# Kernel optimization log

Hardware: AMD Instinct MI355X
Metric: run time of the kernel (lower is better)

## Reference

```python
import jax, jax.numpy as jnp
import numpy as np

MID = 16
HEADS = 8
HEAD_DIM = MID // HEADS  # 2
EPS = 1e-5


def posembed(length, dim):
    # get_posembed_linear: sin-cos 1D positional embedding
    pos = jnp.arange(length, dtype=jnp.float32)
    omega = jnp.arange(dim // 2, dtype=jnp.float32) / (dim / 2.0)
    omega = 1.0 / (10000.0 ** omega)
    out = pos[:, None] * omega[None, :]  # [L, dim//2]
    return jnp.concatenate([jnp.sin(out), jnp.cos(out)], axis=1)  # [L, dim]


def layernorm(x, g, b):
    m = x.mean(-1, keepdims=True)
    v = ((x - m) ** 2).mean(-1, keepdims=True)
    return (x - m) * jax.lax.rsqrt(v + EPS) * g + b


def conv2d(x, w, b):
    # NCHW 3x3 SAME conv
    y = jax.lax.conv_general_dilated(x, w, (1, 1), 'SAME',
                                     dimension_numbers=('NCHW', 'OIHW', 'NCHW'))
    return y + b[None, :, None, None]


def attention(x, wq, wk, wv, wo, bo):
    # diffusers Attention: self-attn, no qkv bias, out bias
    B, S, C = x.shape
    q = (x @ wq.T).reshape(B, S, HEADS, HEAD_DIM)
    k = (x @ wk.T).reshape(B, S, HEADS, HEAD_DIM)
    v = (x @ wv.T).reshape(B, S, HEADS, HEAD_DIM)
    scale = 1.0 / np.sqrt(HEAD_DIM).astype(np.float32)
    scores = jnp.einsum('bshd,bthd->bhst', q, k) * scale
    p = jax.nn.softmax(scores, axis=-1)
    o = jnp.einsum('bhst,bthd->bshd', p, v).reshape(B, S, C)
    return o @ wo.T + bo


def setup_inputs() -> dict:
    key = jax.random.key(0)
    ks = jax.random.split(key, 24)

    def n(k, shape, s=0.05):
        return jax.random.normal(k, shape, dtype=jnp.float32) * s

    b, f, h, w, c = 2, 16, 64, 64, 16
    inp = {
        'hidden_states': n(ks[0], (b, f, h, w, c), 1.0),
        'ref_stats': n(ks[1], (b, f, h, w, c), 1.0),
        'emb': n(ks[2], (b, 512), 1.0),
        'conv_in_w': n(ks[3], (MID, c, 3, 3)),
        'conv_in_b': jnp.zeros((MID,), jnp.float32),
        'emb1_w': n(ks[4], (MID, 512)),
        'emb1_b': jnp.zeros((MID,), jnp.float32),
        'emb2_w': n(ks[5], (MID, MID)),
        'emb2_b': jnp.zeros((MID,), jnp.float32),
        'wqx': n(ks[6], (MID, MID)), 'wkx': n(ks[7], (MID, MID)),
        'wvx': n(ks[8], (MID, MID)), 'wox': n(ks[9], (MID, MID)),
        'box': jnp.zeros((MID,), jnp.float32),
        'wqy': n(ks[10], (MID, MID)), 'wky': n(ks[11], (MID, MID)),
        'wvy': n(ks[12], (MID, MID)), 'woy': n(ks[13], (MID, MID)),
        'boy': jnp.zeros((MID,), jnp.float32),
        'wqt': n(ks[14], (MID, MID)), 'wkt': n(ks[15], (MID, MID)),
        'wvt': n(ks[16], (MID, MID)), 'wot': n(ks[17], (MID, MID)),
        'bot': jnp.zeros((MID,), jnp.float32),
        'norm_g': jnp.ones((MID,), jnp.float32),
        'norm_b': jnp.zeros((MID,), jnp.float32),
        'proj_w': n(ks[18], (c, MID, 3, 3)),  # zero_module in torch; random here so grads flow
        'proj_b': jnp.zeros((c,), jnp.float32),
    }
    return inp


def reference(hidden_states, ref_stats, emb,
              conv_in_w, conv_in_b, emb1_w, emb1_b, emb2_w, emb2_b,
              wqx, wkx, wvx, wox, box,
              wqy, wky, wvy, woy, boy,
              wqt, wkt, wvt, wot, bot,
              norm_g, norm_b, proj_w, proj_b):
    b, f, h, w, c = hidden_states.shape

    # conv stem on (b f) c h w
    x = hidden_states.reshape(b * f, h, w, c).transpose(0, 3, 1, 2)
    x = conv2d(x, conv_in_w, conv_in_b)
    r = ref_stats.reshape(b * f, h, w, c).transpose(0, 3, 1, 2)
    r = conv2d(r, conv_in_w, conv_in_b)

    # TimestepEmbedding: linear -> silu -> linear, broadcast over frames/HW
    e = jax.nn.silu(emb @ emb1_w.T + emb1_b) @ emb2_w.T + emb2_b  # [b, MID]
    r = r + jnp.repeat(e, f, axis=0)[:, :, None, None]

    hs = x.reshape(b, f, MID, h, w).transpose(0, 1, 3, 4, 2)  # b f h w c
    rs = r.reshape(b, f, MID, h, w).transpose(0, 1, 3, 4, 2)

    # row (x) attention: cat along w -> (b f h) 2w c
    cat = jnp.concatenate([hs, rs], axis=3).reshape(b * f * h, 2 * w, MID)
    pe = posembed(2 * w, MID)
    resx = attention(layernorm(cat + pe[None], norm_g, norm_b), wqx, wkx, wvx, wox, box)
    resx = resx[:, :w].reshape(b, f, h, w, MID)

    # column (y) attention: cat along h -> (b f w) 2h c
    cat = jnp.concatenate([resx, rs], axis=2)            # b f 2h w c
    cat = cat.transpose(0, 1, 3, 2, 4).reshape(b * f * w, 2 * h, MID)
    pe = posembed(2 * h, MID)
    resy = attention(layernorm(cat + pe[None], norm_g, norm_b), wqy, wky, wvy, woy, boy)
    resy = resy[:, :h].reshape(b, f, w, h, MID).transpose(0, 1, 3, 2, 4)

    # temporal (t) attention: cat along f -> (b h w) 2f c
    cat = jnp.concatenate([resy, rs], axis=1)            # b 2f h w c
    cat = cat.transpose(0, 2, 3, 1, 4).reshape(b * h * w, 2 * f, MID)
    pe = posembed(2 * f, MID)
    rest = attention(layernorm(cat + pe[None], norm_g, norm_b), wqt, wkt, wvt, wot, bot)
    rest = rest[:, :f].reshape(b, h, w, f, MID).transpose(0, 3, 4, 1, 2).reshape(b * f, MID, h, w)

    out = conv2d(rest, proj_w, proj_b)  # (b f) c h w
    return hidden_states + out.reshape(b, f, c, h, w).transpose(0, 1, 3, 4, 2)
```

## Files before the change

kernel.cpp:

```cpp
#include <hip/hip_runtime.h>
#include <hip/hip_bf16.h>

typedef __hip_bfloat16 bf16;
using hf2 = decltype(__builtin_amdgcn_cvt_pkrtz(0.f, 0.f));
typedef float f32x2 __attribute__((ext_vector_type(2)));
typedef _Float16 v4h __attribute__((ext_vector_type(4)));
typedef float v4f __attribute__((ext_vector_type(4)));

#define BB   2
#define FF   16
#define HH   64
#define WW   64
#define CC   16
#define NIMG (BB*FF)
#define PIX  (HH*WW)
#define IMGSZ (PIX*CC)

#define QSCALE_LOG2E 1.0201394f

__device__ __forceinline__ unsigned pkh2(float a, float b) {
    union { hf2 h; unsigned u; } x;
    x.h = __builtin_amdgcn_cvt_pkrtz(a, b);
    return x.u;
}
__device__ __forceinline__ float fdot2u(unsigned a, unsigned b, float c) {
    union { unsigned u; hf2 h; } A, B;
    A.u = a; B.u = b;
    return __builtin_amdgcn_fdot2(A.h, B.h, c, false);
}
__device__ __forceinline__ f32x2 f2(float a, float b) {
    f32x2 r; r.x = a; r.y = b; return r;
}

__device__ __forceinline__ void ld16f(const float* p, float* x) {
    const float4* p4 = reinterpret_cast<const float4*>(p);
    #pragma unroll
    for (int q = 0; q < 4; ++q) {
        float4 v = p4[q];
        x[4 * q] = v.x; x[4 * q + 1] = v.y; x[4 * q + 2] = v.z; x[4 * q + 3] = v.w;
    }
}

__device__ __forceinline__ unsigned packbf2(float a, float b) {
    union { bf16 h[2]; unsigned u; } pk;
    pk.h[0] = __float2bfloat16(a);
    pk.h[1] = __float2bfloat16(b);
    return pk.u;
}

__device__ __forceinline__ void stage_wB(const float* __restrict__ w,
                                         unsigned* __restrict__ wB, int t) {
    for (int e = t; e < 576; e += 256) {
        int oc = e & 15;
        int c  = (e >> 4) & 3;
        int s  = e >> 6;
        const float* wp = w + (oc * 16 + c * 4) * 9 + s;
        wB[e * 2]     = pkh2(wp[0],  wp[9]);
        wB[e * 2 + 1] = pkh2(wp[18], wp[27]);
    }
}

#define TAP_OFF(s) ((((s) / 3) * 66 + ((s) % 3)) * 12)

__global__ __launch_bounds__(256) void conv_in_kernel(
    const float* __restrict__ hid, const float* __restrict__ ref,
    const float* __restrict__ cw, const float* __restrict__ cb,
    const float* __restrict__ emb,
    const float* __restrict__ e1w, const float* __restrict__ e1b,
    const float* __restrict__ e2w, const float* __restrict__ e2b,
    bf16* __restrict__ A, bf16* __restrict__ R)
{
    __shared__ __align__(16) unsigned stg[6 * 66 * 12];
    __shared__ __align__(16) unsigned wB[1152];
    __shared__ float bl[16], hl[16], el[16];

    int t = threadIdx.x;
    int bid = blockIdx.x;
    int rg   = bid & 15;
    int img2 = bid >> 4;
    int isref = img2 >> 5;
    int img   = img2 & 31;
    int bi    = img >> 4;
    int r0    = rg << 2;

    stage_wB(cw, wB, t);
    if (t < 16) bl[t] = cb[t];

    if (isref) {
        float* red = reinterpret_cast<float*>(stg);
        {
            int o = t >> 4, seg = t & 15;
            const float* er = emb + bi * 512 + seg * 32;
            const float* wr = e1w + o * 512 + seg * 32;
            float p = 0.f;
            #pragma unroll
            for (int k = 0; k < 32; ++k) p = fmaf(er[k], wr[k], p);
            red[t] = p;
        }
        __syncthreads();
        if (t < 16) {
            float acc = e1b[t];
            #pragma unroll
            for (int s = 0; s < 16; ++s) acc += red[t * 16 + s];
            hl[t] = acc / (1.f + __expf(-acc));
        }
        __syncthreads();
        if (t < 16) {
            float acc = e2b[t];
            #pragma unroll
            for (int k = 0; k < 16; ++k) acc = fmaf(hl[k], e2w[t * 16 + k], acc);
            el[t] = acc;
        }
        __syncthreads();
    }

    const float* inp = (isref ? ref : hid) + (size_t)img * IMGSZ;
    for (int s2 = t; s2 < 396; s2 += 256) {
        int rr = s2 / 66, xi = s2 - rr * 66;
        int y = r0 - 1 + rr, px = xi - 1;
        uint4* dst = reinterpret_cast<uint4*>(&stg[(rr * 66 + xi) * 12]);
        if ((unsigned)y < 64u && (unsigned)px < 64u) {
            float xv[16];
            ld16f(inp + (((y << 6) + px) << 4), xv);
            dst[0] = make_uint4(pkh2(xv[0], xv[1]),  pkh2(xv[2], xv[3]),
                                pkh2(xv[4], xv[5]),  pkh2(xv[6], xv[7]));
            dst[1] = make_uint4(pkh2(xv[8], xv[9]),  pkh2(xv[10], xv[11]),
                                pkh2(xv[12], xv[13]), pkh2(xv[14], xv[15]));
        } else {
            dst[0] = make_uint4(0, 0, 0, 0);
            dst[1] = make_uint4(0, 0, 0, 0);
        }
    }
    __syncthreads();

    int l  = t & 63, w = t >> 6;
    int oc = l & 15, c = l >> 4;
    int y  = r0 + w;

    v4h bf[9];
    int cb2 = c * 32 + oc * 2;
    #pragma unroll
    for (int s = 0; s < 9; ++s)
        bf[s] = *reinterpret_cast<const v4h*>(&wB[s * 128 + cb2]);

    float bias = bl[oc] + (isref ? el[oc] : 0.f);
    v4f binit; binit[0] = bias; binit[1] = bias; binit[2] = bias; binit[3] = bias;

    bf16* op = (isref ? R : A) + (size_t)img * IMGSZ;

    #pragma unroll
    for (int xq = 0; xq < 4; ++xq) {
        int ab = (w * 66 + xq * 16 + (l & 15)) * 12 + 2 * c;
        v4f acc = binit;
        #pragma unroll
        for (int s = 0; s < 9; ++s) {
            v4h af = *reinterpret_cast<const v4h*>(&stg[ab + TAP_OFF(s)]);
            acc = __builtin_amdgcn_mfma_f32_16x16x16f16(af, bf[s], acc, 0, 0, 0);
        }
        #pragma unroll
        for (int g = 0; g < 4; ++g) {
            int x = xq * 16 + c * 4 + g;
            op[(((y << 6) + x) << 4) + oc] = __float2bfloat16(acc[g]);
        }
    }
}

template<int S, int SEQPB, int MINW, bool F16OUT>
__global__ __launch_bounds__(256, MINW) void attn_kernel(
    bf16* __restrict__ A, const bf16* __restrict__ R,
    unsigned* __restrict__ A16,
    int d2, int str1, int str2, int tokStride,
    const float* __restrict__ wq, const float* __restrict__ wk,
    const float* __restrict__ wv, const float* __restrict__ wo,
    const float* __restrict__ bo, const float* __restrict__ gw,
    const float* __restrict__ bw)
{
    constexpr int HS  = S / 2;
    constexpr int KQ  = S / 2;
    constexpr int TPT = 256 / (SEQPB * S);
    static_assert(TPT == 2, "all stages use the pair-thread layout");
    constexpr int ITEMS = 256 / SEQPB;
    constexpr int NQG = ITEMS / 16;
    constexpr int QB  = HS / NQG;
    constexpr int QP  = QB / 2;
    constexpr int KROW = 10;
    constexpr int QROW = 20;
    constexpr int KTROW = S + 12;
    constexpr int LSQ = (SEQPB == 1) ? 0 : ((SEQPB == 2) ? 1 : 2);
    constexpr int NW3 = SEQPB * HS * 8 / 256;

    __shared__ float wolT[256];
    __shared__ unsigned wq2L[128], wk2L[128], wv2L[128];
    __shared__ float bol[16], gl[16], blw[16];
    __shared__ __align__(16) unsigned kvT[2 * SEQPB * 8 * KTROW];
    __shared__ __align__(16) unsigned qL[SEQPB * HS * KROW];
    __shared__ int bases[SEQPB];
    unsigned* kT = kvT;
    unsigned* vT = kvT + SEQPB * 8 * KTROW;

    int t = threadIdx.x;
    wolT[(t & 15) * 16 + (t >> 4)] = wo[t];
    if (t < 128) {
        float2 qw = reinterpret_cast<const float2*>(wq)[t];
        float2 kw = reinterpret_cast<const float2*>(wk)[t];
        float2 vw = reinterpret_cast<const float2*>(wv)[t];
        wq2L[t] = pkh2(qw.x * QSCALE_LOG2E, qw.y * QSCALE_LOG2E);
        wk2L[t] = pkh2(kw.x, kw.y);
        wv2L[t] = pkh2(vw.x, vw.y);
    }
    if (t < 16) { bol[t] = bo[t]; gl[t] = gw[t]; blw[t] = bw[t]; }
    if (t < SEQPB) {
        int seq = blockIdx.x * SEQPB + t;
        bases[t] = (seq / d2) * str1 + (seq % d2) * str2;
    }
    __syncthreads();

    const float om[8] = {1.f, 0.31622776601683794f, 0.1f, 0.031622776601683794f,
                         0.01f, 0.0031622776601683794f, 0.001f, 0.00031622776601683794f};

    {
        int tokIdx = t >> 1;
        int half = t & 1;
        int db   = half * 8;
        int sq = tokIdx & (SEQPB - 1);
        int i  = tokIdx >> LSQ;
        const bf16* src = ((i < HS)
            ? (A + bases[sq] + (size_t)i * tokStride)
            : (R + bases[sq] + (size_t)(i - HS) * tokStride)) + db;
        uint4 u = *reinterpret_cast<const uint4*>(src);
        unsigned uu[4] = {u.x, u.y, u.z, u.w};
        float x[8];
        #pragma unroll
        for (int k = 0; k < 4; ++k) {
            union { unsigned u; float f; } lo, hi2;
            lo.u = uu[k] << 16; hi2.u = uu[k] & 0xffff0000u;
            x[2 * k] = lo.f; x[2 * k + 1] = hi2.f;
        }
        float fi = (float)i;
        #pragma unroll
        for (int k = 0; k < 8; ++k) {
            float sv, cv;
            __sincosf(fi * om[k], &sv, &cv);
            x[k] += half ? cv : sv;
        }
        float s8 = 0.f;
        #pragma unroll
        for (int k = 0; k < 8; ++k) s8 += x[k];
        float m = (s8 + __shfl_xor(s8, 1)) * (1.f / 16.f);
        float v8 = 0.f;
        #pragma unroll
        for (int k = 0; k < 8; ++k) { float d = x[k] - m; v8 = fmaf(d, d, v8); }
        float var = (v8 + __shfl_xor(v8, 1)) * (1.f / 16.f);
        float rs = rsqrtf(var + 1e-5f);

        unsigned xpm[4];
        #pragma unroll
        for (int e = 0; e < 4; ++e) {
            float a0 = (x[2 * e]     - m) * rs * gl[db + 2 * e]     + blw[db + 2 * e];
            float a1 = (x[2 * e + 1] - m) * rs * gl[db + 2 * e + 1] + blw[db + 2 * e + 1];
            xpm[e] = pkh2(a0, a1);
        }
        unsigned xp[8];
        #pragma unroll
        for (int e = 0; e < 4; ++e) {
            unsigned oth = __shfl_xor(xpm[e], 1);
            xp[e]     = half ? oth    : xpm[e];
            xp[e + 4] = half ? xpm[e] : oth;
        }
        float qv[8], kv[8], vv[8];
        #pragma unroll
        for (int dd = 0; dd < 8; ++dd) {
            int d = db + dd;
            float aq = 0.f, ak = 0.f, av = 0.f;
            #pragma unroll
            for (int c2 = 0; c2 < 8; ++c2) {
                aq = fdot2u(xp[c2], wq2L[d * 8 + c2], aq);
                ak = fdot2u(xp[c2], wk2L[d * 8 + c2], ak);
                av = fdot2u(xp[c2], wv2L[d * 8 + c2], av);
            }
            qv[dd] = aq; kv[dd] = ak; vv[dd] = av;
        }
        int hb = db >> 1;
        #pragma unroll
        for (int e = 0; e < 4; ++e) {
            int hrow = (sq * 8 + hb + e) * KTROW + i;
            kT[hrow] = pkh2(kv[2 * e], kv[2 * e + 1]);
            vT[hrow] = packbf2(vv[2 * e], vv[2 * e + 1]);
        }
        if (i < HS) {
            uint2* qr = reinterpret_cast<uint2*>(&qL[(sq * HS + i) * KROW + (db >> 1)]);
            #pragma unroll
            for (int e = 0; e < 2; ++e)
                qr[e] = make_uint2(pkh2(qv[4 * e], qv[4 * e + 1]),
                                   pkh2(qv[4 * e + 2], qv[4 * e + 3]));
        }
    }
    __syncthreads();

    int sq2 = t / ITEMS;
    int r   = t % ITEMS;
    int qg  = r >> 4;
    int hd  = (r >> 1) & 7;
    int half2 = r & 1;
    float* oL = reinterpret_cast<float*>(kvT);
    {
        unsigned q2[QB];
        f32x2 l2[QP], a0p[QP], a1p[QP];
        #pragma unroll
        for (int qq = 0; qq < QB; ++qq)
            q2[qq] = qL[(sq2 * HS + qg * QB + qq) * KROW + hd];
        #pragma unroll
        for (int m = 0; m < QP; ++m) {
            l2[m] = f2(0.f, 0.f); a0p[m] = f2(0.f, 0.f); a1p[m] = f2(0.f, 0.f);
        }
        const unsigned* kp = &kT[(sq2 * 8 + hd) * KTROW + half2 * KQ];
        const unsigned* vp = &vT[(sq2 * 8 + hd) * KTROW + half2 * KQ];
        #pragma unroll 4
        for (int jb = 0; jb < KQ / 4; ++jb) {
            uint4 k4 = *reinterpret_cast<const uint4*>(kp + jb * 4);
            uint4 v4 = *reinterpret_cast<const uint4*>(vp + jb * 4);
            unsigned ks[4] = {k4.x, k4.y, k4.z, k4.w};
            unsigned vs[4] = {v4.x, v4.y, v4.z, v4.w};
            #pragma unroll
            for (int e = 0; e < 4; ++e) {
                union { unsigned u; float f; } v0, v1;
                v0.u = vs[e] << 16; v1.u = vs[e] & 0xffff0000u;
                f32x2 v00 = f2(v0.f, v0.f);
                f32x2 v11 = f2(v1.f, v1.f);
                #pragma unroll
                for (int m = 0; m < QP; ++m) {
                    f32x2 p2;
                    p2.x = __builtin_amdgcn_exp2f(fdot2u(q2[2 * m], ks[e], 0.f));
                    p2.y = __builtin_amdgcn_exp2f(fdot2u(q2[2 * m + 1], ks[e], 0.f));
                    l2[m] += p2;
                    a0p[m] = __builtin_elementwise_fma(p2, v00, a0p[m]);
                    a1p[m] = __builtin_elementwise_fma(p2, v11, a1p[m]);
                }
            }
        }
        #pragma unroll
        for (int m = 0; m < QP; ++m) {
            l2[m].x  += __shfl_xor(l2[m].x, 1);  l2[m].y  += __shfl_xor(l2[m].y, 1);
            a0p[m].x += __shfl_xor(a0p[m].x, 1); a0p[m].y += __shfl_xor(a0p[m].y, 1);
            a1p[m].x += __shfl_xor(a1p[m].x, 1); a1p[m].y += __shfl_xor(a1p[m].y, 1);
        }
        __syncthreads();
        if (half2 == 0) {
            #pragma unroll
            for (int m = 0; m < QP; ++m) {
                float inv0 = 1.f / l2[m].x;
                float inv1 = 1.f / l2[m].y;
                *reinterpret_cast<float2*>(
                    &oL[(sq2 * HS + qg * QB + 2 * m) * QROW + 2 * hd]) =
                    make_float2(a0p[m].x * inv0, a1p[m].x * inv0);
                *reinterpret_cast<float2*>(
                    &oL[(sq2 * HS + qg * QB + 2 * m + 1) * QROW + 2 * hd]) =
                    make_float2(a0p[m].y * inv1, a1p[m].y * inv1);
            }
        }
    }
    __syncthreads();

    #pragma unroll
    for (int rep = 0; rep < NW3; ++rep) {
        int idx = t + rep * 256;
        int cp  = idx & 7;
        int g   = idx >> 3;
        int sq3 = g & (SEQPB - 1);
        int tok = g >> LSQ;
        const float* orow = &oL[(sq3 * HS + tok) * QROW];
        float acc0 = bol[2 * cp], acc1 = bol[2 * cp + 1];
        #pragma unroll
        for (int d = 0; d < 16; ++d) {
            acc0 = fmaf(orow[d], wolT[d * 16 + 2 * cp], acc0);
            acc1 = fmaf(orow[d], wolT[d * 16 + 2 * cp + 1], acc1);
        }
        int off = bases[sq3] + tok * tokStride;
        if constexpr (F16OUT)
            A16[(off >> 1) + cp] = pkh2(acc0, acc1);
        else
            *reinterpret_cast<unsigned*>(A + off + 2 * cp) = packbf2(acc0, acc1);
    }
}

__global__ __launch_bounds__(256) void conv_out_kernel(
    const unsigned* __restrict__ A16, const float* __restrict__ hid,
    const float* __restrict__ pw, const float* __restrict__ pb,
    float* __restrict__ out)
{
    __shared__ __align__(16) unsigned stg[4 * 66 * 12];
    __shared__ __align__(16) unsigned wB[1152];
    __shared__ float bl[16];

    int t = threadIdx.x;
    int bid = blockIdx.x;
    int rg  = bid & 31;
    int img = bid >> 5;
    int r0  = rg << 1;

    stage_wB(pw, wB, t);
    if (t < 16) bl[t] = pb[t];

    const unsigned* inp = A16 + ((size_t)img << 15);
    for (int s2 = t; s2 < 264; s2 += 256) {
        int rr = s2 / 66, xi = s2 - rr * 66;
        int y = r0 - 1 + rr, px = xi - 1;
        uint4* dst = reinterpret_cast<uint4*>(&stg[(rr * 66 + xi) * 12]);
        if ((unsigned)y < 64u && (unsigned)px < 64u) {
            const uint4* sp = reinterpret_cast<const uint4*>(
                inp + (((y << 6) + px) << 3));
            dst[0] = sp[0];
            dst[1] = sp[1];
        } else {
            dst[0] = make_uint4(0, 0, 0, 0);
            dst[1] = make_uint4(0, 0, 0, 0);
        }
    }
    __syncthreads();

    int l  = t & 63, w = t >> 6;
    int oc = l & 15, c = l >> 4;

    v4h bf[9];
    int cb2 = c * 32 + oc * 2;
    #pragma unroll
    for (int s = 0; s < 9; ++s)
        bf[s] = *reinterpret_cast<const v4h*>(&wB[s * 128 + cb2]);

    float bias = bl[oc];
    v4f binit; binit[0] = bias; binit[1] = bias; binit[2] = bias; binit[3] = bias;
    size_t obase = (size_t)img * IMGSZ;

    #pragma unroll
    for (int tq = 0; tq < 2; ++tq) {
        int tile = w * 2 + tq;
        int ro = tile >> 2, xq = tile & 3;
        int y  = r0 + ro;
        int ab = (ro * 66 + xq * 16 + (l & 15)) * 12 + 2 * c;
        v4f acc = binit;
        #pragma unroll
        for (int s = 0; s < 9; ++s) {
            v4h af = *reinterpret_cast<const v4h*>(&stg[ab + TAP_OFF(s)]);
            acc = __builtin_amdgcn_mfma_f32_16x16x16f16(af, bf[s], acc, 0, 0, 0);
        }
        #pragma unroll
        for (int g = 0; g < 4; ++g) {
            int x = xq * 16 + c * 4 + g;
            size_t o = obase + (size_t)(((y << 6) + x) << 4) + oc;
            out[o] = acc[g] + hid[o];
        }
    }
}

extern "C" void kernel_launch(void* const* d_in, const int* in_sizes, int n_in,
                              void* d_out, int out_size, void* d_ws, size_t ws_size,
                              hipStream_t stream) {
    const float* hid  = (const float*)d_in[0];
    const float* ref  = (const float*)d_in[1];
    const float* emb  = (const float*)d_in[2];
    const float* ciw  = (const float*)d_in[3];
    const float* cib  = (const float*)d_in[4];
    const float* e1w  = (const float*)d_in[5];
    const float* e1b  = (const float*)d_in[6];
    const float* e2w  = (const float*)d_in[7];
    const float* e2b  = (const float*)d_in[8];
    const float* wqx  = (const float*)d_in[9];
    const float* wkx  = (const float*)d_in[10];
    const float* wvx  = (const float*)d_in[11];
    const float* wox  = (const float*)d_in[12];
    const float* box_ = (const float*)d_in[13];
    const float* wqy  = (const float*)d_in[14];
    const float* wky  = (const float*)d_in[15];
    const float* wvy  = (const float*)d_in[16];
    const float* woy  = (const float*)d_in[17];
    const float* boy  = (const float*)d_in[18];
    const float* wqt  = (const float*)d_in[19];
    const float* wkt  = (const float*)d_in[20];
    const float* wvt  = (const float*)d_in[21];
    const float* wot  = (const float*)d_in[22];
    const float* bot  = (const float*)d_in[23];
    const float* ng   = (const float*)d_in[24];
    const float* nb   = (const float*)d_in[25];
    const float* pjw  = (const float*)d_in[26];
    const float* pjb  = (const float*)d_in[27];

    bf16* A = (bf16*)d_ws;
    unsigned* A16 = (unsigned*)((char*)d_ws + (4 << 20));
    bf16* R = (bf16*)d_out;

    conv_in_kernel<<<2 * NIMG * (HH / 4), 256, 0, stream>>>(
        hid, ref, ciw, cib, emb, e1w, e1b, e2w, e2b, A, R);

    attn_kernel<128, 1, 8, false><<<BB * FF * HH, 256, 0, stream>>>(
        A, R, nullptr, 1, WW * CC, 0, CC, wqx, wkx, wvx, wox, box_, ng, nb);
    attn_kernel<128, 1, 8, false><<<BB * FF * WW, 256, 0, stream>>>(
        A, R, nullptr, WW, IMGSZ, CC, WW * CC, wqy, wky, wvy, woy, boy, ng, nb);
    attn_kernel<32, 4, 8, true><<<(BB * HH * WW) / 4, 256, 0, stream>>>(
        A, R, A16, HH * WW, FF * IMGSZ, CC, IMGSZ, wqt, wkt, wvt, wot, bot, ng, nb);

    conv_out_kernel<<<NIMG * (HH / 2), 256, 0, stream>>>(
        A16, hid, pjw, pjb, (float*)d_out);
}
```

Measured before the change: 224.7 us.

## Fuse input conv and row attention into a single per-row kernel

Merges the conv_in kernel with the x-direction (row) attention stage. Each block convolves one image row of both hidden and reference inputs into LDS as fp16 tokens, then runs layernorm, QKV projection, softmax attention and the output projection in place. The A buffer no longer has to be written and read back from global memory, and one launch goes away. In exchange, each block recomputes the embedding MLP, and the input halo rows are loaded about three times instead of about 1.5 times, since each block now covers one row rather than four.

```diff
diff --git a/kernel.cpp b/kernel.cpp
--- a/kernel.cpp
+++ b/kernel.cpp
@@ -30,6 +30,10 @@
 }
 __device__ __forceinline__ f32x2 f2(float a, float b) {
     f32x2 r; r.x = a; r.y = b; return r;
+}
+__device__ __forceinline__ void unpkh(unsigned u, float& a, float& b) {
+    union { unsigned v; __fp16 h[2]; } x; x.v = u;
+    a = (float)x.h[0]; b = (float)x.h[1];
 }
 
 __device__ __forceinline__ void ld16f(const float* p, float* x) {
@@ -62,106 +66,280 @@
 
 #define TAP_OFF(s) ((((s) / 3) * 66 + ((s) % 3)) * 12)
 
-__global__ __launch_bounds__(256) void conv_in_kernel(
+__global__ __launch_bounds__(256, 6) void cx_kernel(
     const float* __restrict__ hid, const float* __restrict__ ref,
     const float* __restrict__ cw, const float* __restrict__ cb,
     const float* __restrict__ emb,
     const float* __restrict__ e1w, const float* __restrict__ e1b,
     const float* __restrict__ e2w, const float* __restrict__ e2b,
-    bf16* __restrict__ A, bf16* __restrict__ R)
+    bf16* __restrict__ A, bf16* __restrict__ R,
+    const float* __restrict__ wq, const float* __restrict__ wk,
+    const float* __restrict__ wv, const float* __restrict__ wo,
+    const float* __restrict__ bo, const float* __restrict__ gw,
+    const float* __restrict__ bw)
 {
-    __shared__ __align__(16) unsigned stg[6 * 66 * 12];
+    constexpr int HS = 64, KQ = 64;
+    constexpr int QB = 4, QP = 2;
+    constexpr int KROW = 10;
+    constexpr int QROW = 20;
+    constexpr int KTROW = 140;
+
+    __shared__ __align__(16) unsigned stgU[2376];
+    __shared__ __align__(16) unsigned tokL[1024];
     __shared__ __align__(16) unsigned wB[1152];
-    __shared__ float bl[16], hl[16], el[16];
+    __shared__ unsigned wq2L[128], wk2L[128], wv2L[128];
+    __shared__ float wolT[256];
+    __shared__ float bol[16], gl[16], blw[16], bl[16], hl[16], el[16];
 
     int t = threadIdx.x;
-    int bid = blockIdx.x;
-    int rg   = bid & 15;
-    int img2 = bid >> 4;
-    int isref = img2 >> 5;
-    int img   = img2 & 31;
-    int bi    = img >> 4;
-    int r0    = rg << 2;
+    int seq = blockIdx.x;
+    int h   = seq & 63;
+    int img = seq >> 6;
+    int bi  = seq >> 10;
+    int base = img * IMGSZ + h * (WW * CC);
 
     stage_wB(cw, wB, t);
-    if (t < 16) bl[t] = cb[t];
-
-    if (isref) {
-        float* red = reinterpret_cast<float*>(stg);
-        {
-            int o = t >> 4, seg = t & 15;
-            const float* er = emb + bi * 512 + seg * 32;
-            const float* wr = e1w + o * 512 + seg * 32;
-            float p = 0.f;
-            #pragma unroll
-            for (int k = 0; k < 32; ++k) p = fmaf(er[k], wr[k], p);
-            red[t] = p;
-        }
-        __syncthreads();
-        if (t < 16) {
-            float acc = e1b[t];
-            #pragma unroll
-            for (int s = 0; s < 16; ++s) acc += red[t * 16 + s];
-            hl[t] = acc / (1.f + __expf(-acc));
-        }
-        __syncthreads();
-        if (t < 16) {
-            float acc = e2b[t];
-            #pragma unroll
-            for (int k = 0; k < 16; ++k) acc = fmaf(hl[k], e2w[t * 16 + k], acc);
-            el[t] = acc;
-        }
-        __syncthreads();
-    }
-
-    const float* inp = (isref ? ref : hid) + (size_t)img * IMGSZ;
-    for (int s2 = t; s2 < 396; s2 += 256) {
-        int rr = s2 / 66, xi = s2 - rr * 66;
-        int y = r0 - 1 + rr, px = xi - 1;
-        uint4* dst = reinterpret_cast<uint4*>(&stg[(rr * 66 + xi) * 12]);
-        if ((unsigned)y < 64u && (unsigned)px < 64u) {
-            float xv[16];
-            ld16f(inp + (((y << 6) + px) << 4), xv);
-            dst[0] = make_uint4(pkh2(xv[0], xv[1]),  pkh2(xv[2], xv[3]),
-                                pkh2(xv[4], xv[5]),  pkh2(xv[6], xv[7]));
-            dst[1] = make_uint4(pkh2(xv[8], xv[9]),  pkh2(xv[10], xv[11]),
-                                pkh2(xv[12], xv[13]), pkh2(xv[14], xv[15]));
-        } else {
-            dst[0] = make_uint4(0, 0, 0, 0);
-            dst[1] = make_uint4(0, 0, 0, 0);
-        }
-    }
-    __syncthreads();
+    wolT[(t & 15) * 16 + (t >> 4)] = wo[t];
+    if (t < 128) {
+        float2 qw = reinterpret_cast<const float2*>(wq)[t];
+        float2 kw = reinterpret_cast<const float2*>(wk)[t];
+        float2 vw = reinterpret_cast<const float2*>(wv)[t];
+        wq2L[t] = pkh2(qw.x * QSCALE_LOG2E, qw.y * QSCALE_LOG2E);
+        wk2L[t] = pkh2(kw.x, kw.y);
+        wv2L[t] = pkh2(vw.x, vw.y);
+    }
+    if (t < 16) { bol[t] = bo[t]; gl[t] = gw[t]; blw[t] = bw[t]; bl[t] = cb[t]; }
+
+    {
+        float* red = reinterpret_cast<float*>(tokL);
+        int o = t >> 4, seg = t & 15;
+        const float* er = emb + bi * 512 + seg * 32;
+        const float* wr = e1w + o * 512 + seg * 32;
+        float p = 0.f;
+        #pragma unroll
+        for (int k = 0; k < 32; ++k) p = fmaf(er[k], wr[k], p);
+        red[t] = p;
+    }
+    __syncthreads();
+    if (t < 16) {
+        float* red = reinterpret_cast<float*>(tokL);
+        float acc = e1b[t];
+        #pragma unroll
+        for (int s = 0; s < 16; ++s) acc += red[t * 16 + s];
+        hl[t] = acc / (1.f + __expf(-acc));
+    }
+    __syncthreads();
+    if (t < 16) {
+        float acc = e2b[t];
+        #pragma unroll
+        for (int k = 0; k < 16; ++k) acc = fmaf(hl[k], e2w[t * 16 + k], acc);
+        el[t] = acc;
+    }
 
     int l  = t & 63, w = t >> 6;
     int oc = l & 15, c = l >> 4;
-    int y  = r0 + w;
-
-    v4h bf[9];
-    int cb2 = c * 32 + oc * 2;
+    v4h bfr[9];
+    {
+        int cb2 = c * 32 + oc * 2;
+        #pragma unroll
+        for (int s = 0; s < 9; ++s)
+            bfr[s] = *reinterpret_cast<const v4h*>(&wB[s * 128 + cb2]);
+    }
+    __fp16* tok16 = reinterpret_cast<__fp16*>(tokL);
+
     #pragma unroll
-    for (int s = 0; s < 9; ++s)
-        bf[s] = *reinterpret_cast<const v4h*>(&wB[s * 128 + cb2]);
-
-    float bias = bl[oc] + (isref ? el[oc] : 0.f);
-    v4f binit; binit[0] = bias; binit[1] = bias; binit[2] = bias; binit[3] = bias;
-
-    bf16* op = (isref ? R : A) + (size_t)img * IMGSZ;
+    for (int pass = 0; pass < 2; ++pass) {
+        __syncthreads();
+        const float* inp = (pass ? ref : hid) + (size_t)img * IMGSZ;
+        for (int s2 = t; s2 < 198; s2 += 256) {
+            int rr = s2 / 66, xi = s2 - rr * 66;
+            int y = h - 1 + rr, px = xi - 1;
+            uint4* dst = reinterpret_cast<uint4*>(&stgU[(rr * 66 + xi) * 12]);
+            if ((unsigned)y < 64u && (unsigned)px < 64u) {
+                float xv[16];
+                ld16f(inp + (((y << 6) + px) << 4), xv);
+                dst[0] = make_uint4(pkh2(xv[0], xv[1]),  pkh2(xv[2], xv[3]),
+                                    pkh2(xv[4], xv[5]),  pkh2(xv[6], xv[7]));
+                dst[1] = make_uint4(pkh2(xv[8], xv[9]),  pkh2(xv[10], xv[11]),
+                                    pkh2(xv[12], xv[13]), pkh2(xv[14], xv[15]));
+            } else {
+                dst[0] = make_uint4(0, 0, 0, 0);
+                dst[1] = make_uint4(0, 0, 0, 0);
+            }
+        }
+        __syncthreads();
+
+        float bias = bl[oc] + (pass ? el[oc] : 0.f);
+        v4f acc; acc[0] = bias; acc[1] = bias; acc[2] = bias; acc[3] = bias;
+        int ab = ((w << 4) + (l & 15)) * 12 + 2 * c;
+        #pragma unroll
+        for (int s = 0; s < 9; ++s) {
+            v4h af = *reinterpret_cast<const v4h*>(&stgU[ab + TAP_OFF(s)]);
+            acc = __builtin_amdgcn_mfma_f32_16x16x16f16(af, bfr[s], acc, 0, 0, 0);
+        }
+        #pragma unroll
+        for (int g = 0; g < 4; ++g) {
+            int px = (w << 4) + (c << 2) + g;
+            tok16[(pass * 64 + px) * 16 + oc] = (__fp16)acc[g];
+            if (pass)
+                R[base + px * CC + oc] = __float2bfloat16(acc[g]);
+        }
+    }
+    __syncthreads();
+
+    unsigned* kT = stgU;
+    unsigned* vT = stgU + 8 * KTROW;
+
+    const float om[8] = {1.f, 0.31622776601683794f, 0.1f, 0.031622776601683794f,
+                         0.01f, 0.0031622776601683794f, 0.001f, 0.00031622776601683794f};
+
+    __shared__ __align__(16) unsigned qL[HS * KROW];
+    {
+        int i    = t >> 1;
+        int half = t & 1;
+        int db   = half * 8;
+        uint4 u = *reinterpret_cast<const uint4*>(&tokL[i * 8 + half * 4]);
+        unsigned uu[4] = {u.x, u.y, u.z, u.w};
+        float x[8];
+        #pragma unroll
+        for (int k = 0; k < 4; ++k) unpkh(uu[k], x[2 * k], x[2 * k + 1]);
+        float fi = (float)i;
+        #pragma unroll
+        for (int k = 0; k < 8; ++k) {
+            float sv, cv;
+            __sincosf(fi * om[k], &sv, &cv);
+            x[k] += half ? cv : sv;
+        }
+        float s8 = 0.f;
+        #pragma unroll
+        for (int k = 0; k < 8; ++k) s8 += x[k];
+        float m = (s8 + __shfl_xor(s8, 1)) * (1.f / 16.f);
+        float v8 = 0.f;
+        #pragma unroll
+        for (int k = 0; k < 8; ++k) { float d = x[k] - m; v8 = fmaf(d, d, v8); }
+        float var = (v8 + __shfl_xor(v8, 1)) * (1.f / 16.f);
+        float rs = rsqrtf(var + 1e-5f);
+
+        unsigned xpm[4];
+        #pragma unroll
+        for (int e = 0; e < 4; ++e) {
+            float a0 = (x[2 * e]     - m) * rs * gl[db + 2 * e]     + blw[db + 2 * e];
+            float a1 = (x[2 * e + 1] - m) * rs * gl[db + 2 * e + 1] + blw[db + 2 * e + 1];
+            xpm[e] = pkh2(a0, a1);
+        }
+        unsigned xp[8];
+        #pragma unroll
+        for (int e = 0; e < 4; ++e) {
+            unsigned oth = __shfl_xor(xpm[e], 1);
+            xp[e]     = half ? oth    : xpm[e];
+            xp[e + 4] = half ? xpm[e] : oth;
+        }
+        float qv[8], kv[8], vv[8];
+        #pragma unroll
+        for (int dd = 0; dd < 8; ++dd) {
+            int d = db + dd;
+            float aq = 0.f, ak = 0.f, av = 0.f;
+            #pragma unroll
+            for (int c2 = 0; c2 < 8; ++c2) {
+                aq = fdot2u(xp[c2], wq2L[d * 8 + c2], aq);
+                ak = fdot2u(xp[c2], wk2L[d * 8 + c2], ak);
+                av = fdot2u(xp[c2], wv2L[d * 8 + c2], av);
+            }
+            qv[dd] = aq; kv[dd] = ak; vv[dd] = av;
+        }
+        int hb = db >> 1;
+        #pragma unroll
+        for (int e = 0; e < 4; ++e) {
+            int hrow = (hb + e) * KTROW + i;
+            kT[hrow] = pkh2(kv[2 * e], kv[2 * e + 1]);
+            vT[hrow] = packbf2(vv[2 * e], vv[2 * e + 1]);
+        }
+        if (i < HS) {
+            uint2* qr = reinterpret_cast<uint2*>(&qL[i * KROW + (db >> 1)]);
+            #pragma unroll
+            for (int e = 0; e < 2; ++e)
+                qr[e] = make_uint2(pkh2(qv[4 * e], qv[4 * e + 1]),
+                                   pkh2(qv[4 * e + 2], qv[4 * e + 3]));
+        }
+    }
+    __syncthreads();
+
+    int qg  = t >> 4;
+    int hd  = (t >> 1) & 7;
+    int half2 = t & 1;
+    float* oL = reinterpret_cast<float*>(stgU);
+    {
+        unsigned q2[QB];
+        f32x2 l2[QP], a0p[QP], a1p[QP];
+        #pragma unroll
+        for (int qq = 0; qq < QB; ++qq)
+            q2[qq] = qL[(qg * QB + qq) * KROW + hd];
+        #pragma unroll
+        for (int m = 0; m < QP; ++m) {
+            l2[m] = f2(0.f, 0.f); a0p[m] = f2(0.f, 0.f); a1p[m] = f2(0.f, 0.f);
+        }
+        const unsigned* kp = &kT[hd * KTROW + half2 * KQ];
+        const unsigned* vp = &vT[hd * KTROW + half2 * KQ];
+        #pragma unroll 4
+        for (int jb = 0; jb < KQ / 4; ++jb) {
+            uint4 k4 = *reinterpret_cast<const uint4*>(kp + jb * 4);
+            uint4 v4 = *reinterpret_cast<const uint4*>(vp + jb * 4);
+            unsigned ks[4] = {k4.x, k4.y, k4.z, k4.w};
+            unsigned vs[4] = {v4.x, v4.y, v4.z, v4.w};
+            #pragma unroll
+            for (int e = 0; e < 4; ++e) {
+                union { unsigned u; float f; } v0, v1;
+                v0.u = vs[e] << 16; v1.u = vs[e] & 0xffff0000u;
+                f32x2 v00 = f2(v0.f, v0.f);
+                f32x2 v11 = f2(v1.f, v1.f);
+                #pragma unroll
+                for (int m = 0; m < QP; ++m) {
+                    f32x2 p2;
+                    p2.x = __builtin_amdgcn_exp2f(fdot2u(q2[2 * m], ks[e], 0.f));
+                    p2.y = __builtin_amdgcn_exp2f(fdot2u(q2[2 * m + 1], ks[e], 0.f));
+                    l2[m] += p2;
+                    a0p[m] = __builtin_elementwise_fma(p2, v00, a0p[m]);
+                    a1p[m] = __builtin_elementwise_fma(p2, v11, a1p[m]);
+                }
+            }
+        }
+        #pragma unroll
+        for (int m = 0; m < QP; ++m) {
+            l2[m].x  += __shfl_xor(l2[m].x, 1);  l2[m].y  += __shfl_xor(l2[m].y, 1);
+            a0p[m].x += __shfl_xor(a0p[m].x, 1); a0p[m].y += __shfl_xor(a0p[m].y, 1);
+            a1p[m].x += __shfl_xor(a1p[m].x, 1); a1p[m].y += __shfl_xor(a1p[m].y, 1);
+        }
+        __syncthreads();
+        if (half2 == 0) {
+            #pragma unroll
+            for (int m = 0; m < QP; ++m) {
+                float inv0 = 1.f / l2[m].x;
+                float inv1 = 1.f / l2[m].y;
+                *reinterpret_cast<float2*>(
+                    &oL[(qg * QB + 2 * m) * QROW + 2 * hd]) =
+                    make_float2(a0p[m].x * inv0, a1p[m].x * inv0);
+                *reinterpret_cast<float2*>(
+                    &oL[(qg * QB + 2 * m + 1) * QROW + 2 * hd]) =
+                    make_float2(a0p[m].y * inv1, a1p[m].y * inv1);
+            }
+        }
+    }
+    __syncthreads();
 
     #pragma unroll
-    for (int xq = 0; xq < 4; ++xq) {
-        int ab = (w * 66 + xq * 16 + (l & 15)) * 12 + 2 * c;
-        v4f acc = binit;
-        #pragma unroll
-        for (int s = 0; s < 9; ++s) {
-            v4h af = *reinterpret_cast<const v4h*>(&stg[ab + TAP_OFF(s)]);
-            acc = __builtin_amdgcn_mfma_f32_16x16x16f16(af, bf[s], acc, 0, 0, 0);
-        }
-        #pragma unroll
-        for (int g = 0; g < 4; ++g) {
-            int x = xq * 16 + c * 4 + g;
-            op[(((y << 6) + x) << 4) + oc] = __float2bfloat16(acc[g]);
-        }
+    for (int rep = 0; rep < 2; ++rep) {
+        int idx = t + rep * 256;
+        int cp  = idx & 7;
+        int tok = idx >> 3;
+        const float* orow = &oL[tok * QROW];
+        float acc0 = bol[2 * cp], acc1 = bol[2 * cp + 1];
+        #pragma unroll
+        for (int d = 0; d < 16; ++d) {
+            acc0 = fmaf(orow[d], wolT[d * 16 + 2 * cp], acc0);
+            acc1 = fmaf(orow[d], wolT[d * 16 + 2 * cp + 1], acc1);
+        }
+        *reinterpret_cast<unsigned*>(A + base + tok * CC + 2 * cp) =
+            packbf2(acc0, acc1);
     }
 }
 
@@ -488,11 +666,10 @@
     unsigned* A16 = (unsigned*)((char*)d_ws + (4 << 20));
     bf16* R = (bf16*)d_out;
 
-    conv_in_kernel<<<2 * NIMG * (HH / 4), 256, 0, stream>>>(
-        hid, ref, ciw, cib, emb, e1w, e1b, e2w, e2b, A, R);
-
-    attn_kernel<128, 1, 8, false><<<BB * FF * HH, 256, 0, stream>>>(
-        A, R, nullptr, 1, WW * CC, 0, CC, wqx, wkx, wvx, wox, box_, ng, nb);
+    cx_kernel<<<BB * FF * HH, 256, 0, stream>>>(
+        hid, ref, ciw, cib, emb, e1w, e1b, e2w, e2b,
+        A, R, wqx, wkx, wvx, wox, box_, ng, nb);
+
     attn_kernel<128, 1, 8, false><<<BB * FF * WW, 256, 0, stream>>>(
         A, R, nullptr, WW, IMGSZ, CC, WW * CC, wqy, wky, wvy, woy, boy, ng, nb);
     attn_kernel<32, 4, 8, true><<<(BB * HH * WW) / 4, 256, 0, stream>>>(
```

Result: no change. 228.8 us (+1.8%).
